# Kernel optimization log

Hardware: AMD Instinct MI355X
Metric: run time of the kernel (lower is better)

## Reference

```python
import jax, jax.numpy as jnp
import numpy as np

ARITY = 4
DEPTH = 8          # leaves = ARITY**DEPTH = 65536; internal nodes = (4**8-1)//3 = 21845
IN_DIM = 64
MEM = 128
HID = 128


def setup_inputs() -> dict:
    key = jax.random.key(0)
    ks = jax.random.split(key, 20)
    n_leaves = ARITY ** DEPTH
    n_internal = (ARITY ** DEPTH - 1) // (ARITY - 1)
    s = 0.05
    inp = {
        "inputs": jax.random.normal(ks[0], (n_leaves, IN_DIM), jnp.float32),
        "ops": jax.random.randint(ks[1], (n_internal,), 0, 2, jnp.int32),
        # MLP (all bias-free); torch Linear weight layout [out, in]
        "W1": jax.random.normal(ks[2], (MEM, IN_DIM), jnp.float32) * s,
        "W2": jax.random.normal(ks[3], (3 * MEM, MEM), jnp.float32) * s,
        "W3": jax.random.normal(ks[4], (2 * MEM, 3 * MEM), jnp.float32) * s,
        "Wp": jax.random.normal(ks[5], (MEM, 2 * MEM), jnp.float32) * s,
        # ChildSumTreeRNN
        "Wand": jax.random.normal(ks[6], (MEM, MEM), jnp.float32) * s,
        "Wor": jax.random.normal(ks[7], (MEM, MEM), jnp.float32) * s,
        "Rw1": jax.random.normal(ks[8], (HID, MEM), jnp.float32) * s,
        "Rb1": jnp.zeros((HID,), jnp.float32),
        "Rw2": jax.random.normal(ks[9], (HID, HID), jnp.float32) * s,
        "Rb2": jnp.zeros((HID,), jnp.float32),
        "Rw3": jax.random.normal(ks[10], (HID, HID), jnp.float32) * s,
        "Rb3": jnp.zeros((HID,), jnp.float32),
        "Rwp": jax.random.normal(ks[11], (1, HID), jnp.float32) * s,
        "Rbp": jnp.zeros((1,), jnp.float32),
    }
    return inp


def reference(inputs, ops, W1, W2, W3, Wp, Wand, Wor,
              Rw1, Rb1, Rw2, Rb2, Rw3, Rb3, Rwp, Rbp):
    # MLP embedding of all leaves  [n_leaves, MEM]
    h = jnp.tanh(inputs @ W1.T)
    h = jnp.tanh(h @ W2.T)
    h = jnp.tanh(h @ W3.T)
    h = jnp.tanh(h @ Wp.T)

    # ChildSumTreeRNN, level by level (children before parents).
    # Complete arity-4 tree: level l has 4**l internal nodes; ops is
    # level-ordered from the root, so level l starts at (4**l - 1)//3.
    for l in range(DEPTH - 1, -1, -1):
        n = ARITY ** l
        start = (ARITY ** l - 1) // (ARITY - 1)
        ops_l = ops[start:start + n]                      # [n]
        ch = h.reshape(n, ARITY, MEM)                     # children states
        ha = jnp.tanh(jnp.einsum('ncm,om->nco', ch, Wand)).mean(axis=1)
        ho = jnp.tanh(jnp.einsum('ncm,om->nco', ch, Wor)).mean(axis=1)
        h = jnp.where((ops_l == 0)[:, None], ha, ho)      # [n, MEM]

    x = jax.nn.relu(h @ Rw1.T + Rb1)
    x = jax.nn.relu(x @ Rw2.T + Rb2)
    x = jax.nn.relu(x @ Rw3.T + Rb3)
    out = x @ Rwp.T + Rbp                                 # [1, 1]
    return out
```

## Files before the change

kernel.cpp:

```cpp
#include <hip/hip_runtime.h>
#include <hip/hip_bf16.h>
#include <stdint.h>

#define N_LEAVES 65536
#define MEM 128
#define HID 128

typedef float  f32x4 __attribute__((ext_vector_type(4)));
typedef short  s16x8 __attribute__((ext_vector_type(8)));
typedef unsigned short u16;
typedef u16    u16x8 __attribute__((ext_vector_type(8)));

__device__ __forceinline__ u16 f2bf(float x) {
    unsigned u = __builtin_bit_cast(unsigned, x);
    u += 0x7FFFu + ((u >> 16) & 1u);
    return (u16)(u >> 16);
}
__device__ __forceinline__ float bf2f(u16 b) {
    unsigned u = ((unsigned)b) << 16;
    return __builtin_bit_cast(float, u);
}
__device__ __forceinline__ float hif(float x) {
    return __builtin_bit_cast(float, __builtin_bit_cast(unsigned, x) & 0xffff0000u);
}
__device__ __forceinline__ unsigned packbf(float e0, float e1) {
    return __builtin_amdgcn_perm(__builtin_bit_cast(unsigned, e1),
                                 __builtin_bit_cast(unsigned, e0), 0x07060302u);
}
__device__ __forceinline__ float tanh_c(float x) {
    float E = __builtin_amdgcn_exp2f(x * 2.8853900817779268f);
    return 1.0f - 2.0f * __builtin_amdgcn_rcpf(E + 1.0f);
}
__device__ __forceinline__ float tanh_p(float x) {
    float x2 = x * x;
    float poly = x * (1.0f + x2 * (-0.33333334f + x2 * 0.13333334f));
    float E = __builtin_amdgcn_exp2f(x * 2.8853900817779268f);
    float ex = 1.0f - 2.0f * __builtin_amdgcn_rcpf(E + 1.0f);
    return (__builtin_fabsf(x) < 0.25f) ? poly : ex;
}

__device__ __forceinline__ f32x4 mfma_bf(s16x8 a, s16x8 b, f32x4 c) {
    return __builtin_amdgcn_mfma_f32_16x16x32_bf16(a, b, c, 0, 0, 0);
}

__global__ __launch_bounds__(256) void prep_all(
    const float* __restrict__ W1, const float* __restrict__ W2,
    const float* __restrict__ W3, const float* __restrict__ Wp,
    const float* __restrict__ Wand, const float* __restrict__ Wor,
    u16* __restrict__ w1tH, u16* __restrict__ w1tL,
    u16* __restrict__ w2tH, u16* __restrict__ w2tL,
    u16* __restrict__ w3tH, u16* __restrict__ w3tL,
    u16* __restrict__ wptH, u16* __restrict__ wptL,
    u16* __restrict__ waH,  u16* __restrict__ waL,
    u16* __restrict__ woH,  u16* __restrict__ woL)
{
    int g = blockIdx.x * 256 + threadIdx.x;
    const float* W; u16 *Th, *Tl; int K, N, base;
    if (g < 1024)       { W = W1;  Th = w1tH; Tl = w1tL; N = 128; K = 64;  base = 0; }
    else if (g < 7168)  { W = W2;  Th = w2tH; Tl = w2tL; N = 384; K = 128; base = 1024; }
    else if (g < 19456) { W = W3;  Th = w3tH; Tl = w3tL; N = 256; K = 384; base = 7168; }
    else if (g < 23552) { W = Wp;  Th = wptH; Tl = wptL; N = 128; K = 256; base = 19456; }
    else if (g < 25600) { W = Wand; Th = waH; Tl = waL;  N = 128; K = 128; base = 23552; }
    else if (g < 27648) { W = Wor;  Th = woH; Tl = woL;  N = 128; K = 128; base = 25600; }
    else return;
    int t = g - base;
    int kg8 = K >> 3;
    int n = t / kg8, kg = t - n * kg8;
    const float* src = &W[(size_t)n * K + kg * 8];
    size_t dst = ((size_t)kg * N + n) * 8;
    u16x8 hv, lv;
    #pragma unroll
    for (int j = 0; j < 8; ++j) {
        float v = src[j];
        u16 hb = f2bf(v);
        hv[j] = hb;
        lv[j] = f2bf(v - bf2f(hb));
    }
    *(u16x8*)&Th[dst] = hv;
    *(u16x8*)&Tl[dst] = lv;
}

__device__ __forceinline__ int act_g(int Wu, int row, int c4) {
    return row * (Wu >> 3) + (c4 ^ (row & 7));
}

template<int FJ, int KTN, int WIN, int WOUT, bool TOGLOBAL>
__device__ __forceinline__ void mlp_layer_t(
    const u16* inH, const u16* inL,
    const u16* __restrict__ BtH, const u16* __restrict__ BtL,
    u16* outH, u16* outL,
    int gRowBase, int w, int l)
{
    const int lr = l & 15, lc = l >> 4;
    const int featBase = w * (FJ * 16);

    f32x4 acc[FJ][2] = {};
    s16x8 wh[2][FJ], wl[2][FJ];

    #pragma unroll
    for (int fi = 0; fi < FJ; ++fi) {
        int o = (lc * WOUT + featBase + fi * 16 + lr) * 8;
        wh[0][fi] = *(const s16x8*)&BtH[o];
        wl[0][fi] = *(const s16x8*)&BtL[o];
    }

    #pragma unroll
    for (int kt = 0; kt < KTN; ++kt) {
        const int cur = kt & 1;
        if (kt + 1 < KTN) {
            #pragma unroll
            for (int fi = 0; fi < FJ; ++fi) {
                int o = (((kt + 1) * 4 + lc) * WOUT + featBase + fi * 16 + lr) * 8;
                wh[cur ^ 1][fi] = *(const s16x8*)&BtH[o];
                wl[cur ^ 1][fi] = *(const s16x8*)&BtL[o];
            }
        }
        s16x8 ah[2], al[2];
        #pragma unroll
        for (int rj = 0; rj < 2; ++rj) {
            int off = act_g(WIN, rj * 16 + lr, kt * 4 + lc) * 8;
            ah[rj] = *(const s16x8*)&inH[off];
            al[rj] = *(const s16x8*)&inL[off];
        }
        #pragma unroll
        for (int fi = 0; fi < FJ; ++fi)
            #pragma unroll
            for (int rj = 0; rj < 2; ++rj) {
                f32x4 a = acc[fi][rj];
                a = mfma_bf(wh[cur][fi], ah[rj], a);
                a = mfma_bf(wh[cur][fi], al[rj], a);
                a = mfma_bf(wl[cur][fi], ah[rj], a);
                acc[fi][rj] = a;
            }
    }

    #pragma unroll
    for (int fi = 0; fi < FJ; ++fi)
        #pragma unroll
        for (int rj = 0; rj < 2; ++rj) {
            int m  = rj * 16 + lr;
            int n0 = featBase + fi * 16 + lc * 4;
            f32x4 v = acc[fi][rj];
            float t0 = tanh_c(v[0]), t1 = tanh_c(v[1]);
            float t2 = tanh_c(v[2]), t3 = tanh_c(v[3]);
            uint2 hp, lp;
            hp.x = packbf(t0, t1);
            hp.y = packbf(t2, t3);
            lp.x = packbf(t0 - hif(t0), t1 - hif(t1));
            lp.y = packbf(t2 - hif(t2), t3 - hif(t3));
            if constexpr (TOGLOBAL) {
                size_t gaddr = (size_t)(gRowBase + m) * WOUT + n0;
                *(uint2*)&outH[gaddr] = hp;
                *(uint2*)&outL[gaddr] = lp;
            } else {
                int go = act_g(WOUT, m, n0 >> 3) * 8 + (n0 & 7);
                *(uint2*)&outH[go] = hp;
                *(uint2*)&outL[go] = lp;
            }
        }
}

__global__ __launch_bounds__(512, 4) void leaf_fused(
    const float* __restrict__ x,
    const u16* __restrict__ W1tH, const u16* __restrict__ W1tL,
    const u16* __restrict__ W2tH, const u16* __restrict__ W2tL,
    const u16* __restrict__ W3tH, const u16* __restrict__ W3tL,
    const u16* __restrict__ WptH, const u16* __restrict__ WptL,
    u16* __restrict__ h4H, u16* __restrict__ h4L)
{
    __shared__ u16 buf0[2 * 32 * 384];
    __shared__ u16 buf1[2 * 32 * 256];

    const int tid = threadIdx.x;
    const int w = tid >> 6, l = tid & 63;
    const int rowBase = blockIdx.x * 32;

    if (tid < 256) {
        int row = tid >> 3;
        int c0  = (tid & 7) * 8;
        const float* src = &x[(size_t)(rowBase + row) * 64 + c0];
        float4 v0 = *(const float4*)src;
        float4 v1 = *(const float4*)(src + 4);
        float xs[8] = {v0.x, v0.y, v0.z, v0.w, v1.x, v1.y, v1.z, v1.w};
        int go = act_g(64, row, c0 >> 3) * 8;
        uint4 hp, lp;
        hp.x = packbf(xs[0], xs[1]); hp.y = packbf(xs[2], xs[3]);
        hp.z = packbf(xs[4], xs[5]); hp.w = packbf(xs[6], xs[7]);
        lp.x = packbf(xs[0] - hif(xs[0]), xs[1] - hif(xs[1]));
        lp.y = packbf(xs[2] - hif(xs[2]), xs[3] - hif(xs[3]));
        lp.z = packbf(xs[4] - hif(xs[4]), xs[5] - hif(xs[5]));
        lp.w = packbf(xs[6] - hif(xs[6]), xs[7] - hif(xs[7]));
        *(uint4*)&buf0[go] = hp;
        *(uint4*)&buf0[32 * 64 + go] = lp;
    }
    __syncthreads();

    mlp_layer_t<1, 2, 64, 128, false>(buf0, buf0 + 32 * 64, W1tH, W1tL,
                                      buf1, buf1 + 32 * 128, 0, w, l);
    __syncthreads();
    mlp_layer_t<3, 4, 128, 384, false>(buf1, buf1 + 32 * 128, W2tH, W2tL,
                                       buf0, buf0 + 32 * 384, 0, w, l);
    __syncthreads();
    mlp_layer_t<2, 12, 384, 256, false>(buf0, buf0 + 32 * 384, W3tH, W3tL,
                                        buf1, buf1 + 32 * 256, 0, w, l);
    __syncthreads();
    mlp_layer_t<1, 8, 256, 128, true>(buf1, buf1 + 32 * 256, WptH, WptL,
                                      h4H, h4L, rowBase, w, l);
}

template<int CJ, int FJ, bool TOGLOBAL>
__device__ __forceinline__ void tree_level(
    const u16* inH, const u16* inL,
    const u16* __restrict__ wAH, const u16* __restrict__ wAL,
    const u16* __restrict__ wOH, const u16* __restrict__ wOL,
    const int* __restrict__ opsL,
    u16* outH, u16* outL,
    int outRowBase, int nValid, int cfBase, int ffBase, int l)
{
    const int lr = l & 15, lc = l >> 4;
    f32x4 accA[CJ][FJ] = {};
    f32x4 accO[CJ][FJ] = {};

    #pragma unroll
    for (int kt = 0; kt < 4; ++kt) {
        s16x8 ah[CJ], al[CJ];
        #pragma unroll
        for (int c = 0; c < CJ; ++c) {
            int off = act_g(128, (cfBase + c) * 16 + lr, kt * 4 + lc) * 8;
            ah[c] = *(const s16x8*)&inH[off];
            al[c] = *(const s16x8*)&inL[off];
        }
        #pragma unroll
        for (int f = 0; f < FJ; ++f) {
            int wo = ((kt * 4 + lc) * 128 + ffBase + f * 16 + lr) * 8;
            s16x8 bah = *(const s16x8*)&wAH[wo];
            s16x8 bal = *(const s16x8*)&wAL[wo];
            s16x8 boh = *(const s16x8*)&wOH[wo];
            s16x8 bol = *(const s16x8*)&wOL[wo];
            #pragma unroll
            for (int c = 0; c < CJ; ++c) {
                f32x4 a = accA[c][f];
                a = mfma_bf(ah[c], bah, a);
                a = mfma_bf(ah[c], bal, a);
                a = mfma_bf(al[c], bah, a);
                accA[c][f] = a;
                f32x4 o = accO[c][f];
                o = mfma_bf(ah[c], boh, o);
                o = mfma_bf(ah[c], bol, o);
                o = mfma_bf(al[c], boh, o);
                accO[c][f] = o;
            }
        }
    }

    #pragma unroll
    for (int c = 0; c < CJ; ++c) {
        int p = (cfBase + c) * 4 + lc;
        if (p < nValid) {
            int op = opsL[p];
            #pragma unroll
            for (int f = 0; f < FJ; ++f) {
                f32x4 v = op ? accO[c][f] : accA[c][f];
                float t = 0.25f * (tanh_p(v[0]) + tanh_p(v[1]) + tanh_p(v[2]) + tanh_p(v[3]));
                unsigned bits = __builtin_bit_cast(unsigned, t);
                u16 hb = (u16)(bits >> 16);
                float lof = t - __builtin_bit_cast(float, bits & 0xffff0000u);
                u16 lb = (u16)(__builtin_bit_cast(unsigned, lof) >> 16);
                int feat = ffBase + f * 16 + lr;
                if constexpr (TOGLOBAL) {
                    int ga = (outRowBase + p) * 128 + feat;
                    outH[ga] = hb;
                    outL[ga] = lb;
                } else {
                    int go = act_g(128, p, feat >> 3) * 8 + (feat & 7);
                    outH[go] = hb;
                    outL[go] = lb;
                }
            }
        }
    }
}

__global__ __launch_bounds__(512, 4) void tree3(
    const u16* __restrict__ inH, const u16* __restrict__ inL,
    const u16* __restrict__ wAH, const u16* __restrict__ wAL,
    const u16* __restrict__ wOH, const u16* __restrict__ wOL,
    const int* __restrict__ ops0, const int* __restrict__ ops1,
    const int* __restrict__ ops2,
    u16* __restrict__ outH, u16* __restrict__ outL)
{
    __shared__ u16 L0H[16384], L0L[16384];
    __shared__ u16 L1H[4096],  L1L[4096];

    const int tid = threadIdx.x;
    const int w = tid >> 6, l = tid & 63;
    const int blk = blockIdx.x;

    #pragma unroll
    for (int it = 0; it < 4; ++it) {
        int g = tid + it * 512;
        int row = g >> 4, c4 = g & 15;
        size_t src = (size_t)(blk * 128 + row) * 128 + c4 * 8;
        int dst = act_g(128, row, c4) * 8;
        *(u16x8*)&L0H[dst] = *(const u16x8*)&inH[src];
        *(u16x8*)&L0L[dst] = *(const u16x8*)&inL[src];
    }
    __syncthreads();

    tree_level<2, 4, false>(L0H, L0L, wAH, wAL, wOH, wOL, ops0 + blk * 32,
                            L1H, L1L, 0, 32, (w & 3) * 2, (w >> 2) * 64, l);
    __syncthreads();
    tree_level<1, 2, false>(L1H, L1L, wAH, wAL, wOH, wOL, ops1 + blk * 8,
                            L0H, L0L, 0, 8, (w >> 2), (w & 3) * 32, l);
    __syncthreads();
    tree_level<1, 1, true>(L0H, L0L, wAH, wAL, wOH, wOL, ops2 + blk * 2,
                           outH, outL, blk * 2, 2, 0, w * 16, l);
}

__global__ __launch_bounds__(256) void tail_kernel(
    const u16* __restrict__ h2H, const u16* __restrict__ h2L,
    const int* __restrict__ ops,
    const float* __restrict__ Wand, const float* __restrict__ Wor,
    const float* __restrict__ Rw1, const float* __restrict__ Rb1,
    const float* __restrict__ Rw2, const float* __restrict__ Rb2,
    const float* __restrict__ Rw3, const float* __restrict__ Rb3,
    const float* __restrict__ Rwp, const float* __restrict__ Rbp,
    float* __restrict__ out)
{
    __shared__ float H[16 * 128];
    __shared__ float P[4 * 128];
    __shared__ float R[128], X1[128], X2[128], X3[128];
    const int tid = threadIdx.x;

    for (int i = tid; i < 2048; i += 256) H[i] = bf2f(h2H[i]) + bf2f(h2L[i]);
    __syncthreads();

    for (int idx = tid; idx < 512; idx += 256) {
        int p = idx >> 7, o = idx & 127;
        const float* Wsel = (ops[1 + p] == 0) ? Wand : Wor;
        const float4* wr = (const float4*)&Wsel[o * 128];
        const float4* h0 = (const float4*)&H[(p * 4 + 0) * 128];
        const float4* h1 = (const float4*)&H[(p * 4 + 1) * 128];
        const float4* h2 = (const float4*)&H[(p * 4 + 2) * 128];
        const float4* h3 = (const float4*)&H[(p * 4 + 3) * 128];
        float s0 = 0, s1 = 0, s2 = 0, s3 = 0;
        for (int m = 0; m < 32; ++m) {
            float4 wv = wr[m];
            float4 a0 = h0[m], a1 = h1[m], a2 = h2[m], a3 = h3[m];
            s0 += wv.x*a0.x + wv.y*a0.y + wv.z*a0.z + wv.w*a0.w;
            s1 += wv.x*a1.x + wv.y*a1.y + wv.z*a1.z + wv.w*a1.w;
            s2 += wv.x*a2.x + wv.y*a2.y + wv.z*a2.z + wv.w*a2.w;
            s3 += wv.x*a3.x + wv.y*a3.y + wv.z*a3.z + wv.w*a3.w;
        }
        P[idx] = 0.25f * (tanh_p(s0) + tanh_p(s1) + tanh_p(s2) + tanh_p(s3));
    }
    __syncthreads();

    if (tid < 128) {
        int o = tid;
        const float* Wsel = (ops[0] == 0) ? Wand : Wor;
        const float4* wr = (const float4*)&Wsel[o * 128];
        const float4* h0 = (const float4*)&P[0];
        const float4* h1 = (const float4*)&P[128];
        const float4* h2 = (const float4*)&P[256];
        const float4* h3 = (const float4*)&P[384];
        float s0 = 0, s1 = 0, s2 = 0, s3 = 0;
        for (int m = 0; m < 32; ++m) {
            float4 wv = wr[m];
            float4 a0 = h0[m], a1 = h1[m], a2 = h2[m], a3 = h3[m];
            s0 += wv.x*a0.x + wv.y*a0.y + wv.z*a0.z + wv.w*a0.w;
            s1 += wv.x*a1.x + wv.y*a1.y + wv.z*a1.z + wv.w*a1.w;
            s2 += wv.x*a2.x + wv.y*a2.y + wv.z*a2.z + wv.w*a2.w;
            s3 += wv.x*a3.x + wv.y*a3.y + wv.z*a3.z + wv.w*a3.w;
        }
        R[o] = 0.25f * (tanh_p(s0) + tanh_p(s1) + tanh_p(s2) + tanh_p(s3));
    }
    __syncthreads();

    if (tid < 128) {
        const float4* wr = (const float4*)&Rw1[tid * 128];
        const float4* xr = (const float4*)&R[0];
        float s = 0;
        for (int m = 0; m < 32; ++m) {
            float4 wv = wr[m], xv = xr[m];
            s += wv.x*xv.x + wv.y*xv.y + wv.z*xv.z + wv.w*xv.w;
        }
        X1[tid] = fmaxf(s + Rb1[tid], 0.f);
    }
    __syncthreads();
    if (tid < 128) {
        const float4* wr = (const float4*)&Rw2[tid * 128];
        const float4* xr = (const float4*)&X1[0];
        float s = 0;
        for (int m = 0; m < 32; ++m) {
            float4 wv = wr[m], xv = xr[m];
            s += wv.x*xv.x + wv.y*xv.y + wv.z*xv.z + wv.w*xv.w;
        }
        X2[tid] = fmaxf(s + Rb2[tid], 0.f);
    }
    __syncthreads();
    if (tid < 128) {
        const float4* wr = (const float4*)&Rw3[tid * 128];
        const float4* xr = (const float4*)&X2[0];
        float s = 0;
        for (int m = 0; m < 32; ++m) {
            float4 wv = wr[m], xv = xr[m];
            s += wv.x*xv.x + wv.y*xv.y + wv.z*xv.z + wv.w*xv.w;
        }
        X3[tid] = fmaxf(s + Rb3[tid], 0.f) * Rwp[tid];
    }
    __syncthreads();
    if (tid == 0) {
        float t = 0.f;
        for (int i = 0; i < 128; ++i) t += X3[i];
        out[0] = t + Rbp[0];
    }
}

extern "C" void kernel_launch(void* const* d_in, const int* in_sizes, int n_in,
                              void* d_out, int out_size, void* d_ws, size_t ws_size,
                              hipStream_t stream)
{
    const float* inputs = (const float*)d_in[0];
    const int*   ops    = (const int*)d_in[1];
    const float* W1     = (const float*)d_in[2];
    const float* W2     = (const float*)d_in[3];
    const float* W3     = (const float*)d_in[4];
    const float* Wp     = (const float*)d_in[5];
    const float* Wand   = (const float*)d_in[6];
    const float* Wor    = (const float*)d_in[7];
    const float* Rw1    = (const float*)d_in[8];
    const float* Rb1    = (const float*)d_in[9];
    const float* Rw2    = (const float*)d_in[10];
    const float* Rb2    = (const float*)d_in[11];
    const float* Rw3    = (const float*)d_in[12];
    const float* Rb3    = (const float*)d_in[13];
    const float* Rwp    = (const float*)d_in[14];
    const float* Rbp    = (const float*)d_in[15];
    float* out = (float*)d_out;
    u16* ws = (u16*)d_ws;

    size_t off = 0;
    u16* w1tH = ws + off; off += 8192;   u16* w1tL = ws + off; off += 8192;
    u16* w2tH = ws + off; off += 49152;  u16* w2tL = ws + off; off += 49152;
    u16* w3tH = ws + off; off += 98304;  u16* w3tL = ws + off; off += 98304;
    u16* wptH = ws + off; off += 32768;  u16* wptL = ws + off; off += 32768;
    u16* waH  = ws + off; off += 16384;  u16* waL  = ws + off; off += 16384;
    u16* woH  = ws + off; off += 16384;  u16* woL  = ws + off; off += 16384;
    u16* h4H  = ws + off; off += (size_t)N_LEAVES * 128;
    u16* h4L  = ws + off; off += (size_t)N_LEAVES * 128;
    u16* l5H  = ws + off; off += 1024 * 128;
    u16* l5L  = ws + off; off += 1024 * 128;
    u16* l2H  = ws + off; off += 16 * 128;
    u16* l2L  = ws + off; off += 16 * 128;

    prep_all<<<108, 256, 0, stream>>>(W1, W2, W3, Wp, Wand, Wor,
        w1tH, w1tL, w2tH, w2tL, w3tH, w3tL, wptH, wptL, waH, waL, woH, woL);

    leaf_fused<<<N_LEAVES / 32, 512, 0, stream>>>(
        inputs, w1tH, w1tL, w2tH, w2tL, w3tH, w3tL, wptH, wptL, h4H, h4L);

    tree3<<<512, 512, 0, stream>>>(h4H, h4L, waH, waL, woH, woL,
        ops + 5461, ops + 1365, ops + 341, l5H, l5L);

    tree3<<<8, 512, 0, stream>>>(l5H, l5L, waH, waL, woH, woL,
        ops + 85, ops + 21, ops + 5, l2H, l2L);

    tail_kernel<<<1, 256, 0, stream>>>(l2H, l2L, ops, Wand, Wor,
        Rw1, Rb1, Rw2, Rb2, Rw3, Rb3, Rwp, Rbp, out);
}
```

Baseline: 155.3 us.

## Fuse first tree level into leaf MLP kernel and merge upper levels into tail

The leaf MLP kernel now keeps its final 32-row output in shared memory and immediately computes the first tree level (8 parents per block), writing only level-7 states to global memory. This avoids a write and re-read of the full 65536x128 leaf embedding. The tree3 pass is shifted to cover levels 6-4, and a new single-block tail kernel computes levels 3-0 with MFMA tree_level calls before the regressor. That removes one kernel launch but puts more serial work on a single block.

Measured after the change: 162.3 us. 1.05x slower.

```diff
diff --git a/kernel.cpp b/kernel.cpp
--- a/kernel.cpp
+++ b/kernel.cpp
@@ -84,12 +84,12 @@
     return row * (Wu >> 3) + (c4 ^ (row & 7));
 }
 
-template<int FJ, int KTN, int WIN, int WOUT, bool TOGLOBAL>
+template<int FJ, int KTN, int WIN, int WOUT>
 __device__ __forceinline__ void mlp_layer_t(
     const u16* inH, const u16* inL,
     const u16* __restrict__ BtH, const u16* __restrict__ BtL,
     u16* outH, u16* outL,
-    int gRowBase, int w, int l)
+    int w, int l)
 {
     const int lr = l & 15, lc = l >> 4;
     const int featBase = w * (FJ * 16);
@@ -148,64 +148,10 @@
             hp.y = packbf(t2, t3);
             lp.x = packbf(t0 - hif(t0), t1 - hif(t1));
             lp.y = packbf(t2 - hif(t2), t3 - hif(t3));
-            if constexpr (TOGLOBAL) {
-                size_t gaddr = (size_t)(gRowBase + m) * WOUT + n0;
-                *(uint2*)&outH[gaddr] = hp;
-                *(uint2*)&outL[gaddr] = lp;
-            } else {
-                int go = act_g(WOUT, m, n0 >> 3) * 8 + (n0 & 7);
-                *(uint2*)&outH[go] = hp;
-                *(uint2*)&outL[go] = lp;
-            }
-        }
-}
-
-__global__ __launch_bounds__(512, 4) void leaf_fused(
-    const float* __restrict__ x,
-    const u16* __restrict__ W1tH, const u16* __restrict__ W1tL,
-    const u16* __restrict__ W2tH, const u16* __restrict__ W2tL,
-    const u16* __restrict__ W3tH, const u16* __restrict__ W3tL,
-    const u16* __restrict__ WptH, const u16* __restrict__ WptL,
-    u16* __restrict__ h4H, u16* __restrict__ h4L)
-{
-    __shared__ u16 buf0[2 * 32 * 384];
-    __shared__ u16 buf1[2 * 32 * 256];
-
-    const int tid = threadIdx.x;
-    const int w = tid >> 6, l = tid & 63;
-    const int rowBase = blockIdx.x * 32;
-
-    if (tid < 256) {
-        int row = tid >> 3;
-        int c0  = (tid & 7) * 8;
-        const float* src = &x[(size_t)(rowBase + row) * 64 + c0];
-        float4 v0 = *(const float4*)src;
-        float4 v1 = *(const float4*)(src + 4);
-        float xs[8] = {v0.x, v0.y, v0.z, v0.w, v1.x, v1.y, v1.z, v1.w};
-        int go = act_g(64, row, c0 >> 3) * 8;
-        uint4 hp, lp;
-        hp.x = packbf(xs[0], xs[1]); hp.y = packbf(xs[2], xs[3]);
-        hp.z = packbf(xs[4], xs[5]); hp.w = packbf(xs[6], xs[7]);
-        lp.x = packbf(xs[0] - hif(xs[0]), xs[1] - hif(xs[1]));
-        lp.y = packbf(xs[2] - hif(xs[2]), xs[3] - hif(xs[3]));
-        lp.z = packbf(xs[4] - hif(xs[4]), xs[5] - hif(xs[5]));
-        lp.w = packbf(xs[6] - hif(xs[6]), xs[7] - hif(xs[7]));
-        *(uint4*)&buf0[go] = hp;
-        *(uint4*)&buf0[32 * 64 + go] = lp;
-    }
-    __syncthreads();
-
-    mlp_layer_t<1, 2, 64, 128, false>(buf0, buf0 + 32 * 64, W1tH, W1tL,
-                                      buf1, buf1 + 32 * 128, 0, w, l);
-    __syncthreads();
-    mlp_layer_t<3, 4, 128, 384, false>(buf1, buf1 + 32 * 128, W2tH, W2tL,
-                                       buf0, buf0 + 32 * 384, 0, w, l);
-    __syncthreads();
-    mlp_layer_t<2, 12, 384, 256, false>(buf0, buf0 + 32 * 384, W3tH, W3tL,
-                                        buf1, buf1 + 32 * 256, 0, w, l);
-    __syncthreads();
-    mlp_layer_t<1, 8, 256, 128, true>(buf1, buf1 + 32 * 256, WptH, WptL,
-                                      h4H, h4L, rowBase, w, l);
+            int go = act_g(WOUT, m, n0 >> 3) * 8 + (n0 & 7);
+            *(uint2*)&outH[go] = hp;
+            *(uint2*)&outL[go] = lp;
+        }
 }
 
 template<int CJ, int FJ, bool TOGLOBAL>
@@ -272,13 +218,69 @@
                     outH[ga] = hb;
                     outL[ga] = lb;
                 } else {
-                    int go = act_g(128, p, feat >> 3) * 8 + (feat & 7);
+                    int go = act_g(128, outRowBase + p, feat >> 3) * 8 + (feat & 7);
                     outH[go] = hb;
                     outL[go] = lb;
                 }
             }
         }
     }
+}
+
+__global__ __launch_bounds__(512, 4) void leaf_fused(
+    const float* __restrict__ x,
+    const u16* __restrict__ W1tH, const u16* __restrict__ W1tL,
+    const u16* __restrict__ W2tH, const u16* __restrict__ W2tL,
+    const u16* __restrict__ W3tH, const u16* __restrict__ W3tL,
+    const u16* __restrict__ WptH, const u16* __restrict__ WptL,
+    const u16* __restrict__ waH,  const u16* __restrict__ waL,
+    const u16* __restrict__ woH,  const u16* __restrict__ woL,
+    const int* __restrict__ ops,
+    u16* __restrict__ l7H, u16* __restrict__ l7L)
+{
+    __shared__ u16 buf0[2 * 32 * 384];
+    __shared__ u16 buf1[2 * 32 * 256];
+
+    const int tid = threadIdx.x;
+    const int w = tid >> 6, l = tid & 63;
+    const int blk = blockIdx.x;
+    const int rowBase = blk * 32;
+
+    if (tid < 256) {
+        int row = tid >> 3;
+        int c0  = (tid & 7) * 8;
+        const float* src = &x[(size_t)(rowBase + row) * 64 + c0];
+        float4 v0 = *(const float4*)src;
+        float4 v1 = *(const float4*)(src + 4);
+        float xs[8] = {v0.x, v0.y, v0.z, v0.w, v1.x, v1.y, v1.z, v1.w};
+        int go = act_g(64, row, c0 >> 3) * 8;
+        uint4 hp, lp;
+        hp.x = packbf(xs[0], xs[1]); hp.y = packbf(xs[2], xs[3]);
+        hp.z = packbf(xs[4], xs[5]); hp.w = packbf(xs[6], xs[7]);
+        lp.x = packbf(xs[0] - hif(xs[0]), xs[1] - hif(xs[1]));
+        lp.y = packbf(xs[2] - hif(xs[2]), xs[3] - hif(xs[3]));
+        lp.z = packbf(xs[4] - hif(xs[4]), xs[5] - hif(xs[5]));
+        lp.w = packbf(xs[6] - hif(xs[6]), xs[7] - hif(xs[7]));
+        *(uint4*)&buf0[go] = hp;
+        *(uint4*)&buf0[32 * 64 + go] = lp;
+    }
+    __syncthreads();
+
+    mlp_layer_t<1, 2, 64, 128>(buf0, buf0 + 32 * 64, W1tH, W1tL,
+                               buf1, buf1 + 32 * 128, w, l);
+    __syncthreads();
+    mlp_layer_t<3, 4, 128, 384>(buf1, buf1 + 32 * 128, W2tH, W2tL,
+                                buf0, buf0 + 32 * 384, w, l);
+    __syncthreads();
+    mlp_layer_t<2, 12, 384, 256>(buf0, buf0 + 32 * 384, W3tH, W3tL,
+                                 buf1, buf1 + 32 * 256, w, l);
+    __syncthreads();
+    mlp_layer_t<1, 8, 256, 128>(buf1, buf1 + 32 * 256, WptH, WptL,
+                                buf0, buf0 + 32 * 128, w, l);
+    __syncthreads();
+    tree_level<2, 1, true>(buf0, buf0 + 32 * 128, waH, waL, woH, woL,
+                           ops + 5461 + blk * 8, l7H, l7L,
+                           blk * 8, 8, 0, w * 16, l);
 }
 
 __global__ __launch_bounds__(512, 4) void tree3(
@@ -317,102 +319,102 @@
                            outH, outL, blk * 2, 2, 0, w * 16, l);
 }
 
-__global__ __launch_bounds__(256) void tail_kernel(
-    const u16* __restrict__ h2H, const u16* __restrict__ h2L,
+__global__ __launch_bounds__(512) void tree_tail(
+    const u16* __restrict__ l4H, const u16* __restrict__ l4L,
     const int* __restrict__ ops,
-    const float* __restrict__ Wand, const float* __restrict__ Wor,
+    const u16* __restrict__ wAH, const u16* __restrict__ wAL,
+    const u16* __restrict__ wOH, const u16* __restrict__ wOL,
     const float* __restrict__ Rw1, const float* __restrict__ Rb1,
     const float* __restrict__ Rw2, const float* __restrict__ Rb2,
     const float* __restrict__ Rw3, const float* __restrict__ Rb3,
     const float* __restrict__ Rwp, const float* __restrict__ Rbp,
     float* __restrict__ out)
 {
-    __shared__ float H[16 * 128];
-    __shared__ float P[4 * 128];
-    __shared__ float R[128], X1[128], X2[128], X3[128];
+    __shared__ u16 LH[16384], LL[16384];
+    __shared__ u16 OH[8192],  OL[8192];
+    __shared__ float F[4 * 128];
+
     const int tid = threadIdx.x;
-
-    for (int i = tid; i < 2048; i += 256) H[i] = bf2f(h2H[i]) + bf2f(h2L[i]);
-    __syncthreads();
-
-    for (int idx = tid; idx < 512; idx += 256) {
-        int p = idx >> 7, o = idx & 127;
-        const float* Wsel = (ops[1 + p] == 0) ? Wand : Wor;
-        const float4* wr = (const float4*)&Wsel[o * 128];
-        const float4* h0 = (const float4*)&H[(p * 4 + 0) * 128];
-        const float4* h1 = (const float4*)&H[(p * 4 + 1) * 128];
-        const float4* h2 = (const float4*)&H[(p * 4 + 2) * 128];
-        const float4* h3 = (const float4*)&H[(p * 4 + 3) * 128];
-        float s0 = 0, s1 = 0, s2 = 0, s3 = 0;
-        for (int m = 0; m < 32; ++m) {
-            float4 wv = wr[m];
-            float4 a0 = h0[m], a1 = h1[m], a2 = h2[m], a3 = h3[m];
-            s0 += wv.x*a0.x + wv.y*a0.y + wv.z*a0.z + wv.w*a0.w;
-            s1 += wv.x*a1.x + wv.y*a1.y + wv.z*a1.z + wv.w*a1.w;
-            s2 += wv.x*a2.x + wv.y*a2.y + wv.z*a2.z + wv.w*a2.w;
-            s3 += wv.x*a3.x + wv.y*a3.y + wv.z*a3.z + wv.w*a3.w;
-        }
-        P[idx] = 0.25f * (tanh_p(s0) + tanh_p(s1) + tanh_p(s2) + tanh_p(s3));
-    }
-    __syncthreads();
-
-    if (tid < 128) {
-        int o = tid;
-        const float* Wsel = (ops[0] == 0) ? Wand : Wor;
-        const float4* wr = (const float4*)&Wsel[o * 128];
-        const float4* h0 = (const float4*)&P[0];
-        const float4* h1 = (const float4*)&P[128];
-        const float4* h2 = (const float4*)&P[256];
-        const float4* h3 = (const float4*)&P[384];
-        float s0 = 0, s1 = 0, s2 = 0, s3 = 0;
-        for (int m = 0; m < 32; ++m) {
-            float4 wv = wr[m];
-            float4 a0 = h0[m], a1 = h1[m], a2 = h2[m], a3 = h3[m];
-            s0 += wv.x*a0.x + wv.y*a0.y + wv.z*a0.z + wv.w*a0.w;
-            s1 += wv.x*a1.x + wv.y*a1.y + wv.z*a1.z + wv.w*a1.w;
-            s2 += wv.x*a2.x + wv.y*a2.y + wv.z*a2.z + wv.w*a2.w;
-            s3 += wv.x*a3.x + wv.y*a3.y + wv.z*a3.z + wv.w*a3.w;
-        }
-        R[o] = 0.25f * (tanh_p(s0) + tanh_p(s1) + tanh_p(s2) + tanh_p(s3));
-    }
-    __syncthreads();
-
+    const int w = tid >> 6, l = tid & 63;
+
+    #pragma unroll
+    for (int it = 0; it < 4; ++it) {
+        int g = tid + it * 512;
+        int row = g >> 4, c4 = g & 15;
+        size_t src = (size_t)row * 128 + c4 * 8;
+        int dst = act_g(128, row, c4) * 8;
+        *(u16x8*)&LH[dst] = *(const u16x8*)&l4H[src];
+        *(u16x8*)&LL[dst] = *(const u16x8*)&l4L[src];
+    }
+    __syncthreads();
+    tree_level<1, 8, false>(LH, LL, wAH, wAL, wOH, wOL, ops + 21,
+                            OH, OL, 0, 32, w, 0, l);
+    __syncthreads();
+
+    #pragma unroll
+    for (int it = 0; it < 4; ++it) {
+        int g = tid + it * 512;
+        int row = g >> 4, c4 = g & 15;
+        size_t src = (size_t)(128 + row) * 128 + c4 * 8;
+        int dst = act_g(128, row, c4) * 8;
+        *(u16x8*)&LH[dst] = *(const u16x8*)&l4H[src];
+        *(u16x8*)&LL[dst] = *(const u16x8*)&l4L[src];
+    }
+    __syncthreads();
+    tree_level<1, 8, false>(LH, LL, wAH, wAL, wOH, wOL, ops + 21 + 32,
+                            OH, OL, 32, 32, w, 0, l);
+    __syncthreads();
+
+    tree_level<1, 4, false>(OH, OL, wAH, wAL, wOH, wOL, ops + 5,
+                            LH, LL, 0, 16, (w & 3), (w >> 2) * 64, l);
+    __syncthreads();
+
+    tree_level<1, 1, false>(LH, LL, wAH, wAL, wOH, wOL, ops + 1,
+                            OH, OL, 0, 4, 0, w * 16, l);
+    __syncthreads();
+
+    tree_level<1, 1, false>(OH, OL, wAH, wAL, wOH, wOL, ops + 0,
+                            LH, LL, 0, 1, 0, w * 16, l);
+    __syncthreads();
+
+    if (tid < 128) F[tid] = bf2f(LH[tid]) + bf2f(LL[tid]);
+    __syncthreads();
     if (tid < 128) {
         const float4* wr = (const float4*)&Rw1[tid * 128];
-        const float4* xr = (const float4*)&R[0];
+        const float4* xr = (const float4*)&F[0];
         float s = 0;
         for (int m = 0; m < 32; ++m) {
             float4 wv = wr[m], xv = xr[m];
             s += wv.x*xv.x + wv.y*xv.y + wv.z*xv.z + wv.w*xv.w;
         }
-        X1[tid] = fmaxf(s + Rb1[tid], 0.f);
+        F[128 + tid] = fmaxf(s + Rb1[tid], 0.f);
     }
     __syncthreads();
     if (tid < 128) {
         const float4* wr = (const float4*)&Rw2[tid * 128];
-        const float4* xr = (const float4*)&X1[0];
+        const float4* xr = (const float4*)&F[128];
         float s = 0;
         for (int m = 0; m < 32; ++m) {
             float4 wv = wr[m], xv = xr[m];
             s += wv.x*xv.x + wv.y*xv.y + wv.z*xv.z + wv.w*xv.w;
         }
-        X2[tid] = fmaxf(s + Rb2[tid], 0.f);
+        F[256 + tid] = fmaxf(s + Rb2[tid], 0.f);
     }
     __syncthreads();
     if (tid < 128) {
         const float4* wr = (const float4*)&Rw3[tid * 128];
-        const float4* xr = (const float4*)&X2[0];
+        const float4* xr = (const float4*)&F[256];
         float s = 0;
         for (int m = 0; m < 32; ++m) {
             float4 wv = wr[m], xv = xr[m];
             s += wv.x*xv.x + wv.y*xv.y + wv.z*xv.z + wv.w*xv.w;
         }
-        X3[tid] = fmaxf(s + Rb3[tid], 0.f) * Rwp[tid];
+        F[384 + tid] = fmaxf(s + Rb3[tid], 0.f) * Rwp[tid];
     }
     __syncthreads();
     if (tid == 0) {
         float t = 0.f;
-        for (int i = 0; i < 128; ++i) t += X3[i];
+        for (int i = 0; i < 128; ++i) t += F[384 + i];
         out[0] = t + Rbp[0];
     }
 }
@@ -447,25 +449,21 @@
     u16* wptH = ws + off; off += 32768;  u16* wptL = ws + off; off += 32768;
     u16* waH  = ws + off; off += 16384;  u16* waL  = ws + off; off += 16384;
     u16* woH  = ws + off; off += 16384;  u16* woL  = ws + off; off += 16384;
-    u16* h4H  = ws + off; off += (size_t)N_LEAVES * 128;
-    u16* h4L  = ws + off; off += (size_t)N_LEAVES * 128;
-    u16* l5H  = ws + off; off += 1024 * 128;
-    u16* l5L  = ws + off; off += 1024 * 128;
-    u16* l2H  = ws + off; off += 16 * 128;
-    u16* l2L  = ws + off; off += 16 * 128;
+    u16* l7H  = ws + off; off += (size_t)16384 * 128;
+    u16* l7L  = ws + off; off += (size_t)16384 * 128;
+    u16* l4H  = ws + off; off += 256 * 128;
+    u16* l4L  = ws + off; off += 256 * 128;
 
     prep_all<<<108, 256, 0, stream>>>(W1, W2, W3, Wp, Wand, Wor,
         w1tH, w1tL, w2tH, w2tL, w3tH, w3tL, wptH, wptL, waH, waL, woH, woL);
 
     leaf_fused<<<N_LEAVES / 32, 512, 0, stream>>>(
-        inputs, w1tH, w1tL, w2tH, w2tL, w3tH, w3tL, wptH, wptL, h4H, h4L);
-
-    tree3<<<512, 512, 0, stream>>>(h4H, h4L, waH, waL, woH, woL,
-        ops + 5461, ops + 1365, ops + 341, l5H, l5L);
-
-    tree3<<<8, 512, 0, stream>>>(l5H, l5L, waH, waL, woH, woL,
-        ops + 85, ops + 21, ops + 5, l2H, l2L);
-
-    tail_kernel<<<1, 256, 0, stream>>>(l2H, l2L, ops, Wand, Wor,
+        inputs, w1tH, w1tL, w2tH, w2tL, w3tH, w3tL, wptH, wptL,
+        waH, waL, woH, woL, ops, l7H, l7L);
+
+    tree3<<<128, 512, 0, stream>>>(l7H, l7L, waH, waL, woH, woL,
+        ops + 1365, ops + 341, ops + 85, l4H, l4L);
+
+    tree_tail<<<1, 512, 0, stream>>>(l4H, l4L, ops, waH, waL, woH, woL,
         Rw1, Rb1, Rw2, Rb2, Rw3, Rb3, Rwp, Rbp, out);
 }
```
